# Optimization experiments

Hardware: AMD Instinct MI355X
Metric: run time of the kernel (lower is better)

The kernel has to match this reference:

```python
import jax, jax.numpy as jnp
import numpy as np

N = 500000
E = 500000
F = 128
BN_EPS = 1e-3


def setup_inputs() -> dict:
    key = jax.random.key(0)
    ks = jax.random.split(key, 8)
    return {
        "x": jax.random.normal(ks[0], (N, F), dtype=jnp.float32),
        "pairs_prev": jax.random.randint(ks[1], (E, 2), 0, N, dtype=jnp.int64),
        "pairs_next": jax.random.randint(ks[2], (E, 2), 0, N, dtype=jnp.int64),
        "w_next": jax.random.normal(ks[3], (F, F), dtype=jnp.float32),
        "w_prev": jax.random.normal(ks[4], (F, F), dtype=jnp.float32),
        "b": jnp.zeros((1, F), dtype=jnp.float32),
        "bn_gamma": jnp.ones((F,), dtype=jnp.float32),
        "bn_beta": jnp.zeros((F,), dtype=jnp.float32),
        "gru_kernel": jax.random.normal(ks[5], (F, 3 * F), dtype=jnp.float32) * 0.1,
        "gru_rec_kernel": jax.random.normal(ks[6], (F, 3 * F), dtype=jnp.float32) * 0.1,
        "gru_bias": jax.random.normal(ks[7], (2, 3 * F), dtype=jnp.float32) * 0.1,
    }


def _gru(x, h, kernel, rec_kernel, bias, hidden):
    matrix_x = x @ kernel + bias[0]            # (N, 3H)
    x_z, x_r, x_h = jnp.split(matrix_x, 3, axis=-1)
    matrix_inner = h @ rec_kernel + bias[1]    # (N, 3H)
    rec_z, rec_r, rec_h = jnp.split(matrix_inner, 3, axis=-1)
    z = jax.nn.sigmoid(x_z + rec_z)
    r = jax.nn.sigmoid(x_r + rec_r)
    h_cand = jnp.tanh(x_h + r * rec_h)
    return z * h + (1.0 - z) * h_cand


def reference(x, pairs_prev, pairs_next, w_next, w_prev, b,
              bn_gamma, bn_beta, gru_kernel, gru_rec_kernel, gru_bias):
    num_nodes = x.shape[0]
    # gather source-node features, scatter-add onto target nodes
    prev_sumx = jax.ops.segment_sum(x[pairs_prev[:, 1]], pairs_prev[:, 0],
                                    num_segments=num_nodes)
    next_sumx = jax.ops.segment_sum(x[pairs_next[:, 1]], pairs_next[:, 0],
                                    num_segments=num_nodes)
    aggre = next_sumx @ w_next + prev_sumx @ w_prev + b
    aggre = aggre + x  # multiply=None -> residual skip
    # BatchNorm1d (training mode): batch mean / biased variance over nodes
    a = jax.nn.relu(aggre)
    mean = jnp.mean(a, axis=0)
    var = jnp.mean((a - mean) ** 2, axis=0)
    a = (a - mean) * jax.lax.rsqrt(var + BN_EPS) * bn_gamma + bn_beta
    return _gru(a, x, gru_kernel, gru_rec_kernel, gru_bias, x.shape[1])
```

## Files before the change

kernel.cpp:

```cpp
#include <hip/hip_runtime.h>
#include <hip/hip_bf16.h>

#define N_NODES 500000
#define E_EDGES 500000
#define FDIM 128
#define BN_EPS 1e-3f
#define OFFS 500001
#define GCAP 64

#define WS_BUCKETS 0
#define WS_SCALESHIFT 16384
#define WS_PW 16640
#define WS_PW2 65792
#define WS_XBF 82176

#define SO_CNT 0
#define SO_OFF 1000000
#define SO_PART 2100000
#define SO_CUR 2200000
#define SO_SRC 3200000

typedef __attribute__((ext_vector_type(4))) float v4f;
typedef __attribute__((ext_vector_type(8))) __bf16 v8bf;

__device__ __forceinline__ unsigned f2bf_u(float f) {
  unsigned u = __float_as_uint(f);
  return ((u + 0x7FFF + ((u >> 16) & 1)) >> 16) & 0xFFFF;
}
__device__ __forceinline__ unsigned f2bf2(float a, float b) {
  return f2bf_u(a) | (f2bf_u(b) << 16);
}
__device__ __forceinline__ float bf2f(unsigned short u) {
  return __uint_as_float((unsigned)u << 16);
}
__device__ __forceinline__ float fast_sigmoid(float x) {
  float e = __expf(-x);
  return __builtin_amdgcn_rcpf(1.f + e);
}
__device__ __forceinline__ float fast_tanh(float x) {
  x = fminf(fmaxf(x, -15.f), 15.f);
  float e = __expf(2.f * x);
  return (e - 1.f) * __builtin_amdgcn_rcpf(e + 1.f);
}

__global__ __launch_bounds__(256) void repack_gru(
    const float* __restrict__ gk, const float* __restrict__ rk,
    unsigned short* __restrict__ pw) {
  int idx = blockIdx.x * 256 + threadIdx.x;
  int side = idx / 49152;
  int rem = idx % 49152;
  int gate = rem >> 14;
  int rr = rem & 16383;
  int c = rr >> 7, k = rr & 127;
  const float* src = side ? rk : gk;
  float v = src[k * 384 + gate * 128 + c];
  int w = c >> 5, nb = (c >> 4) & 1, l15 = c & 15;
  int ks = k >> 5, lg = (k >> 3) & 3, j = k & 7;
  int lane = lg * 16 + l15;
  int e = w * 24576 + ks * 6144 + nb * 3072 + gate * 1024 + side * 512 + lane * 8 + j;
  pw[e] = (unsigned short)f2bf_u(v);
}

__global__ __launch_bounds__(256) void repack_w(
    const float* __restrict__ w_next, const float* __restrict__ w_prev,
    unsigned short* __restrict__ pw2) {
  int idx = blockIdx.x * 256 + threadIdx.x;
  int side = idx >> 14;
  int rr = idx & 16383;
  int c = rr >> 7, k = rr & 127;
  const float* src = side ? w_prev : w_next;
  float v = src[k * 128 + c];
  int nh = c >> 6, nb = (c >> 4) & 3, l15 = c & 15;
  int ks = k >> 5, lg = (k >> 3) & 3, j = k & 7;
  int lane = lg * 16 + l15;
  int e = nh * 16384 + ks * 4096 + nb * 1024 + side * 512 + lane * 8 + j;
  pw2[e] = (unsigned short)f2bf_u(v);
}

__global__ __launch_bounds__(256) void xbf_kernel(const float* __restrict__ x,
                                                  unsigned short* __restrict__ xbf) {
  size_t i = ((size_t)blockIdx.x * 256 + threadIdx.x) * 8;
  if (i >= (size_t)N_NODES * FDIM) return;
  float4 a = *(const float4*)(x + i);
  float4 b = *(const float4*)(x + i + 4);
  uint4 o = make_uint4(f2bf2(a.x, a.y), f2bf2(a.z, a.w), f2bf2(b.x, b.y),
                       f2bf2(b.z, b.w));
  *(uint4*)(xbf + i) = o;
}

__global__ __launch_bounds__(256) void hist_kernel(const int* __restrict__ pp,
                                                   const int* __restrict__ pn,
                                                   unsigned* __restrict__ cnt) {
  int i = blockIdx.x * 256 + threadIdx.x;
  if (i >= 2 * E_EDGES) return;
  int side = i >= E_EDGES;
  const int* pair = side ? pn + 2 * (i - E_EDGES) : pp + 2 * i;
  atomicAdd(&cnt[side * N_NODES + pair[0]], 1u);
}

__global__ __launch_bounds__(256) void scan1_kernel(const unsigned* __restrict__ cnt,
                                                    unsigned* __restrict__ off,
                                                    unsigned* __restrict__ part) {
  __shared__ unsigned ls[256];
  int side = blockIdx.y;
  int b = blockIdx.x;
  int td = threadIdx.x;
  int base = b * 1024 + td * 4;
  const unsigned* c = cnt + (size_t)side * N_NODES;
  unsigned v0 = 0, v1 = 0, v2 = 0, v3 = 0;
  if (base + 3 < N_NODES) {
    v0 = c[base]; v1 = c[base + 1]; v2 = c[base + 2]; v3 = c[base + 3];
  } else {
    if (base < N_NODES) v0 = c[base];
    if (base + 1 < N_NODES) v1 = c[base + 1];
    if (base + 2 < N_NODES) v2 = c[base + 2];
  }
  unsigned s = v0 + v1 + v2 + v3;
  ls[td] = s;
  __syncthreads();
  unsigned run = s;
  for (int st = 1; st < 256; st <<= 1) {
    unsigned o = (td >= st) ? ls[td - st] : 0u;
    __syncthreads();
    run += o;
    ls[td] = run;
    __syncthreads();
  }
  unsigned excl = run - s;
  unsigned* oo = off + (size_t)side * OFFS;
  if (base < N_NODES) oo[base] = excl;
  if (base + 1 < N_NODES) oo[base + 1] = excl + v0;
  if (base + 2 < N_NODES) oo[base + 2] = excl + v0 + v1;
  if (base + 3 < N_NODES) oo[base + 3] = excl + v0 + v1 + v2;
  if (td == 255) part[side * 512 + b] = run;
}

__global__ __launch_bounds__(1024) void scan2_kernel(unsigned* __restrict__ part) {
  __shared__ unsigned ls[1024];
  int td = threadIdx.x;
  int b = td & 511;
  unsigned s = part[td];
  ls[td] = s;
  __syncthreads();
  unsigned run = s;
  for (int st = 1; st < 512; st <<= 1) {
    unsigned o = (b >= st) ? ls[td - st] : 0u;
    __syncthreads();
    run += o;
    ls[td] = run;
    __syncthreads();
  }
  part[td] = run - s;
}

__global__ __launch_bounds__(256) void scan3_kernel(unsigned* __restrict__ off,
                                                    const unsigned* __restrict__ part,
                                                    unsigned* __restrict__ cur) {
  int side = blockIdx.y;
  int i = blockIdx.x * 256 + threadIdx.x;
  if (i < N_NODES) {
    unsigned v = off[(size_t)side * OFFS + i] + part[side * 512 + (i >> 10)];
    off[(size_t)side * OFFS + i] = v;
    cur[(size_t)side * N_NODES + i] = v;
  }
  if (i == 0) off[(size_t)side * OFFS + N_NODES] = E_EDGES;
}

__global__ __launch_bounds__(256) void reorder_kernel(const int* __restrict__ pp,
                                                      const int* __restrict__ pn,
                                                      unsigned* __restrict__ cur,
                                                      unsigned* __restrict__ srcbuf) {
  int i = blockIdx.x * 256 + threadIdx.x;
  if (i >= 2 * E_EDGES) return;
  int side = i >= E_EDGES;
  const int* pair = side ? pn + 2 * (i - E_EDGES) : pp + 2 * i;
  unsigned pos = atomicAdd(&cur[(size_t)side * N_NODES + pair[0]], 1u);
  srcbuf[(size_t)side * E_EDGES + pos] = (unsigned)pair[1];
}

__global__ __launch_bounds__(256) void aggre_fused(
    const unsigned short* __restrict__ xbf, const unsigned* __restrict__ off,
    const unsigned* __restrict__ srcbuf, const unsigned short* __restrict__ pw2,
    const float* __restrict__ b, unsigned short* __restrict__ a_out,
    float* __restrict__ buckets) {
  __shared__ unsigned short Ap[32 * 128];
  __shared__ unsigned short An[32 * 128];
  __shared__ unsigned short stage[GCAP][128];
  __shared__ unsigned soff[33];
  __shared__ unsigned ssrc[GCAP];
  __shared__ float rs[2][128];
  __shared__ float rq[2][128];
  int t = threadIdx.x;
  int r0 = blockIdx.x * 32;
  int rr = t >> 3, fc = t & 7;

  for (int side = 0; side < 2; ++side) {
    const unsigned* oo = off + (size_t)side * OFFS + r0;
    if (t < 33) soff[t] = oo[t];
    __syncthreads();
    unsigned e0 = soff[0], e1 = soff[32];
    const unsigned* sl = srcbuf + (size_t)side * E_EDGES;
    float acc[16];
#pragma unroll
    for (int i = 0; i < 16; ++i) acc[i] = 0.f;

    for (unsigned base = e0; base < e1; base += GCAP) {
      unsigned cnt = (e1 - base) < (unsigned)GCAP ? (e1 - base) : (unsigned)GCAP;
      if (t < cnt) ssrc[t] = sl[base + t];
      __syncthreads();
      int g = t >> 5, ld = t & 31;
      for (unsigned j = g; j < cnt; j += 8) {
        size_t s = ssrc[j];
        uint2 v = *(const uint2*)(xbf + s * FDIM + ld * 4);
        *(uint2*)&stage[j][ld * 4] = v;
      }
      __syncthreads();
      unsigned rsb = soff[rr] > base ? soff[rr] : base;
      unsigned reb = soff[rr + 1] < base + cnt ? soff[rr + 1] : base + cnt;
      for (unsigned i = rsb; i < reb; ++i) {
        uint4 u0 = *(const uint4*)&stage[i - base][fc * 16];
        uint4 u1 = *(const uint4*)&stage[i - base][fc * 16 + 8];
        acc[0] += bf2f((unsigned short)(u0.x & 0xffff)); acc[1] += __uint_as_float(u0.x & 0xffff0000u);
        acc[2] += bf2f((unsigned short)(u0.y & 0xffff)); acc[3] += __uint_as_float(u0.y & 0xffff0000u);
        acc[4] += bf2f((unsigned short)(u0.z & 0xffff)); acc[5] += __uint_as_float(u0.z & 0xffff0000u);
        acc[6] += bf2f((unsigned short)(u0.w & 0xffff)); acc[7] += __uint_as_float(u0.w & 0xffff0000u);
        acc[8] += bf2f((unsigned short)(u1.x & 0xffff)); acc[9] += __uint_as_float(u1.x & 0xffff0000u);
        acc[10] += bf2f((unsigned short)(u1.y & 0xffff)); acc[11] += __uint_as_float(u1.y & 0xffff0000u);
        acc[12] += bf2f((unsigned short)(u1.z & 0xffff)); acc[13] += __uint_as_float(u1.z & 0xffff0000u);
        acc[14] += bf2f((unsigned short)(u1.w & 0xffff)); acc[15] += __uint_as_float(u1.w & 0xffff0000u);
      }
      __syncthreads();
    }
    unsigned short* dstl = side ? An : Ap;
    int b0 = (rr * 256 + fc * 32) ^ ((rr & 7) << 4);
    int b1 = (rr * 256 + fc * 32 + 16) ^ ((rr & 7) << 4);
    uint4 o0 = make_uint4(f2bf2(acc[0], acc[1]), f2bf2(acc[2], acc[3]),
                          f2bf2(acc[4], acc[5]), f2bf2(acc[6], acc[7]));
    uint4 o1 = make_uint4(f2bf2(acc[8], acc[9]), f2bf2(acc[10], acc[11]),
                          f2bf2(acc[12], acc[13]), f2bf2(acc[14], acc[15]));
    *(uint4*)((char*)dstl + b0) = o0;
    *(uint4*)((char*)dstl + b1) = o1;
    __syncthreads();
  }

  int w = t >> 6, lane = t & 63;
  int m0 = (w & 1) * 16, nh = w >> 1;
  int l15 = lane & 15, lg = lane >> 4;

  v4f acc[4];
#pragma unroll
  for (int nb = 0; nb < 4; ++nb) acc[nb] = (v4f){0.f, 0.f, 0.f, 0.f};

#pragma unroll
  for (int ks = 0; ks < 4; ++ks) {
    int mm = m0 + l15;
    int byte = (mm * 256 + ks * 64 + lg * 16) ^ ((mm & 7) << 4);
    v8bf ap = __builtin_bit_cast(v8bf, *(const uint4*)((const char*)Ap + byte));
    v8bf an = __builtin_bit_cast(v8bf, *(const uint4*)((const char*)An + byte));
    const unsigned short* wb = pw2 + nh * 16384 + ks * 4096 + lane * 8;
#pragma unroll
    for (int nb = 0; nb < 4; ++nb) {
      v8bf bn_ = __builtin_bit_cast(v8bf, *(const uint4*)(wb + nb * 1024));
      v8bf bp_ = __builtin_bit_cast(v8bf, *(const uint4*)(wb + nb * 1024 + 512));
      acc[nb] = __builtin_amdgcn_mfma_f32_16x16x32_bf16(an, bn_, acc[nb], 0, 0, 0);
      acc[nb] = __builtin_amdgcn_mfma_f32_16x16x32_bf16(ap, bp_, acc[nb], 0, 0, 0);
    }
  }

  float s1[4], s2[4];
#pragma unroll
  for (int nb = 0; nb < 4; ++nb) {
    int c = nh * 64 + nb * 16 + l15;
    float bb = b[c];
    s1[nb] = 0.f;
    s2[nb] = 0.f;
#pragma unroll
    for (int r = 0; r < 4; ++r) {
      int row = r0 + m0 + 4 * lg + r;
      size_t o = (size_t)row * FDIM + c;
      float v = acc[nb][r] + bb + bf2f(xbf[o]);
      v = fmaxf(v, 0.f);
      a_out[o] = (unsigned short)f2bf_u(v);
      s1[nb] += v;
      s2[nb] += v * v;
    }
    s1[nb] += __shfl_xor(s1[nb], 16);
    s1[nb] += __shfl_xor(s1[nb], 32);
    s2[nb] += __shfl_xor(s2[nb], 16);
    s2[nb] += __shfl_xor(s2[nb], 32);
  }
  if (lane < 16) {
#pragma unroll
    for (int nb = 0; nb < 4; ++nb) {
      rs[w & 1][nh * 64 + nb * 16 + lane] = s1[nb];
      rq[w & 1][nh * 64 + nb * 16 + lane] = s2[nb];
    }
  }
  __syncthreads();
  if (t < 128) {
    float s = rs[0][t] + rs[1][t];
    float q = rq[0][t] + rq[1][t];
    float* bkt = buckets + (size_t)(blockIdx.x & 63) * 256;
    atomicAdd(bkt + t, s);
    atomicAdd(bkt + 128 + t, q);
  }
}

__global__ void bn_finalize(const float* __restrict__ buckets,
                            const float* __restrict__ gamma,
                            const float* __restrict__ beta,
                            float* __restrict__ scaleshift) {
  int t = threadIdx.x;
  float s = 0.f, q = 0.f;
  for (int j = 0; j < 64; ++j) {
    s += buckets[j * 256 + t];
    q += buckets[j * 256 + 128 + t];
  }
  float mean = s / (float)N_NODES;
  float var = q / (float)N_NODES - mean * mean;
  var = fmaxf(var, 0.f);
  float sc = gamma[t] * rsqrtf(var + BN_EPS);
  scaleshift[t] = sc;
  scaleshift[128 + t] = beta[t] - mean * sc;
}

__global__ __launch_bounds__(256) void gru_mfma(
    const unsigned short* __restrict__ a_bf, const unsigned short* __restrict__ xbf,
    const unsigned short* __restrict__ pw, const float* __restrict__ gbias,
    const float* __restrict__ scaleshift, float* __restrict__ out) {
  __shared__ unsigned short Aa[32 * 128];
  __shared__ unsigned short Ax[32 * 128];
  int t = threadIdx.x;
  int r0 = blockIdx.x * 32;

#pragma unroll
  for (int i = 0; i < 2; ++i) {
    int q = t + 256 * i;
    int row = q >> 4, kq = q & 15;
    size_t g = (size_t)(r0 + row) * FDIM + kq * 8;
    uint4 av = *(const uint4*)(a_bf + g);
    uint4 xv = *(const uint4*)(xbf + g);
    float4 sc0 = *(const float4*)(scaleshift + kq * 8);
    float4 sc1 = *(const float4*)(scaleshift + kq * 8 + 4);
    float4 sh0 = *(const float4*)(scaleshift + 128 + kq * 8);
    float4 sh1 = *(const float4*)(scaleshift + 128 + kq * 8 + 4);
    float a0 = __uint_as_float(av.x << 16), a1 = __uint_as_float(av.x & 0xffff0000u);
    float a2 = __uint_as_float(av.y << 16), a3 = __uint_as_float(av.y & 0xffff0000u);
    float a4 = __uint_as_float(av.z << 16), a5 = __uint_as_float(av.z & 0xffff0000u);
    float a6 = __uint_as_float(av.w << 16), a7 = __uint_as_float(av.w & 0xffff0000u);
    uint4 na = make_uint4(f2bf2(a0 * sc0.x + sh0.x, a1 * sc0.y + sh0.y),
                          f2bf2(a2 * sc0.z + sh0.z, a3 * sc0.w + sh0.w),
                          f2bf2(a4 * sc1.x + sh1.x, a5 * sc1.y + sh1.y),
                          f2bf2(a6 * sc1.z + sh1.z, a7 * sc1.w + sh1.w));
    int byte = (row * 256 + kq * 16) ^ ((row & 7) << 4);
    *(uint4*)((char*)Aa + byte) = na;
    *(uint4*)((char*)Ax + byte) = xv;
  }
  __syncthreads();

  int w = t >> 6, lane = t & 63;
  int l15 = lane & 15, lg = lane >> 4;

  v4f az[2][2], ar[2][2], ah0[2][2], ah1[2][2];
#pragma unroll
  for (int m = 0; m < 2; ++m)
#pragma unroll
    for (int nb = 0; nb < 2; ++nb) {
      az[m][nb] = (v4f){0.f, 0.f, 0.f, 0.f};
      ar[m][nb] = (v4f){0.f, 0.f, 0.f, 0.f};
      ah0[m][nb] = (v4f){0.f, 0.f, 0.f, 0.f};
      ah1[m][nb] = (v4f){0.f, 0.f, 0.f, 0.f};
    }

#pragma unroll
  for (int ks = 0; ks < 4; ++ks) {
    v8bf aa[2], ax[2];
#pragma unroll
    for (int m = 0; m < 2; ++m) {
      int mm = m * 16 + l15;
      int byte = (mm * 256 + ks * 64 + lg * 16) ^ ((mm & 7) << 4);
      aa[m] = __builtin_bit_cast(v8bf, *(const uint4*)((const char*)Aa + byte));
      ax[m] = __builtin_bit_cast(v8bf, *(const uint4*)((const char*)Ax + byte));
    }
    const unsigned short* wb = pw + w * 24576 + ks * 6144 + lane * 8;
#pragma unroll
    for (int nb = 0; nb < 2; ++nb) {
      const unsigned short* wn = wb + nb * 3072;
      v8bf b0z = __builtin_bit_cast(v8bf, *(const uint4*)(wn));
      v8bf b1z = __builtin_bit_cast(v8bf, *(const uint4*)(wn + 512));
      v8bf b0r = __builtin_bit_cast(v8bf, *(const uint4*)(wn + 1024));
      v8bf b1r = __builtin_bit_cast(v8bf, *(const uint4*)(wn + 1536));
      v8bf b0h = __builtin_bit_cast(v8bf, *(const uint4*)(wn + 2048));
      v8bf b1h = __builtin_bit_cast(v8bf, *(const uint4*)(wn + 2560));
#pragma unroll
      for (int m = 0; m < 2; ++m) {
        az[m][nb] = __builtin_amdgcn_mfma_f32_16x16x32_bf16(aa[m], b0z, az[m][nb], 0, 0, 0);
        az[m][nb] = __builtin_amdgcn_mfma_f32_16x16x32_bf16(ax[m], b1z, az[m][nb], 0, 0, 0);
        ar[m][nb] = __builtin_amdgcn_mfma_f32_16x16x32_bf16(aa[m], b0r, ar[m][nb], 0, 0, 0);
        ar[m][nb] = __builtin_amdgcn_mfma_f32_16x16x32_bf16(ax[m], b1r, ar[m][nb], 0, 0, 0);
        ah0[m][nb] = __builtin_amdgcn_mfma_f32_16x16x32_bf16(aa[m], b0h, ah0[m][nb], 0, 0, 0);
        ah1[m][nb] = __builtin_amdgcn_mfma_f32_16x16x32_bf16(ax[m], b1h, ah1[m][nb], 0, 0, 0);
      }
    }
  }

#pragma unroll
  for (int nb = 0; nb < 2; ++nb) {
    int c = w * 32 + nb * 16 + l15;
    float bz = gbias[c] + gbias[384 + c];
    float br = gbias[128 + c] + gbias[512 + c];
    float bh0 = gbias[256 + c];
    float bh1 = gbias[640 + c];
#pragma unroll
    for (int m = 0; m < 2; ++m) {
#pragma unroll
      for (int r = 0; r < 4; ++r) {
        int rl = m * 16 + 4 * lg + r;
        int row = r0 + rl;
        float z = fast_sigmoid(az[m][nb][r] + bz);
        float rg = fast_sigmoid(ar[m][nb][r] + br);
        float hc = fast_tanh(ah0[m][nb][r] + bh0 + rg * (ah1[m][nb][r] + bh1));
        int hb = (rl * 256 + c * 2) ^ ((rl & 7) << 4);
        float h = bf2f(*(const unsigned short*)((const char*)Ax + hb));
        __builtin_nontemporal_store(z * h + (1.f - z) * hc,
                                    out + (size_t)row * FDIM + c);
      }
    }
  }
}

extern "C" void kernel_launch(void* const* d_in, const int* in_sizes, int n_in,
                              void* d_out, int out_size, void* d_ws, size_t ws_size,
                              hipStream_t stream) {
  const float* x = (const float*)d_in[0];
  const int* pp = (const int*)d_in[1];
  const int* pn = (const int*)d_in[2];
  const float* w_next = (const float*)d_in[3];
  const float* w_prev = (const float*)d_in[4];
  const float* b = (const float*)d_in[5];
  const float* gamma = (const float*)d_in[6];
  const float* beta = (const float*)d_in[7];
  const float* gk = (const float*)d_in[8];
  const float* rk = (const float*)d_in[9];
  const float* gbias = (const float*)d_in[10];
  float* out = (float*)d_out;
  float* ws = (float*)d_ws;

  float* buckets = ws + WS_BUCKETS;
  float* scaleshift = ws + WS_SCALESHIFT;
  unsigned short* pw = (unsigned short*)(ws + WS_PW);
  unsigned short* pw2 = (unsigned short*)(ws + WS_PW2);
  unsigned short* xbf = (unsigned short*)(ws + WS_XBF);
  unsigned short* a_bf = xbf + (size_t)N_NODES * FDIM;

  unsigned* u = (unsigned*)d_out;
  unsigned* cnt = u + SO_CNT;
  unsigned* off = u + SO_OFF;
  unsigned* part = u + SO_PART;
  unsigned* cur = u + SO_CUR;
  unsigned* srcbuf = u + SO_SRC;

  hipMemsetAsync(cnt, 0, 2u * N_NODES * sizeof(unsigned), stream);
  hipMemsetAsync(part, 0, 1024 * sizeof(unsigned), stream);
  hipMemsetAsync(buckets, 0, (16384 + 256) * sizeof(float), stream);

  repack_gru<<<384, 256, 0, stream>>>(gk, rk, pw);
  repack_w<<<128, 256, 0, stream>>>(w_next, w_prev, pw2);
  xbf_kernel<<<31250, 256, 0, stream>>>(x, xbf);

  hist_kernel<<<(2 * E_EDGES + 255) / 256, 256, 0, stream>>>(pp, pn, cnt);
  scan1_kernel<<<dim3(489, 2), 256, 0, stream>>>(cnt, off, part);
  scan2_kernel<<<1, 1024, 0, stream>>>(part);
  scan3_kernel<<<dim3((N_NODES + 255) / 256, 2), 256, 0, stream>>>(off, part, cur);
  reorder_kernel<<<(2 * E_EDGES + 255) / 256, 256, 0, stream>>>(pp, pn, cur, srcbuf);

  aggre_fused<<<N_NODES / 32, 256, 0, stream>>>(xbf, off, srcbuf, pw2, b, a_bf,
                                                buckets);
  bn_finalize<<<1, 128, 0, stream>>>(buckets, gamma, beta, scaleshift);
  gru_mfma<<<N_NODES / 32, 256, 0, stream>>>(a_bf, xbf, pw, gbias, scaleshift, out);
}
```

Measured before the change: 552.1 us.

## Gather neighbor rows directly per thread and fuse histogram into bf16 conversion

The aggregation kernel drops its shared-memory staging of gathered source rows, the chunked index loads and their barriers. Each thread group of 8 now reads the source-row indices for its own node and loads 32-byte slices of each neighbor row straight from global memory into registers. Both sides' offsets are loaded once before the loop, leaving a single barrier ahead of the MFMA stage. The edge histogram is also merged into the x-to-bf16 conversion kernel, saving one launch, at the cost of less coalesced per-row gathers and uneven per-thread work.

```diff
diff --git a/kernel.cpp b/kernel.cpp
--- a/kernel.cpp
+++ b/kernel.cpp
@@ -6,7 +6,6 @@
 #define FDIM 128
 #define BN_EPS 1e-3f
 #define OFFS 500001
-#define GCAP 64
 
 #define WS_BUCKETS 0
 #define WS_SCALESHIFT 16384
@@ -77,25 +76,24 @@
   pw2[e] = (unsigned short)f2bf_u(v);
 }
 
-__global__ __launch_bounds__(256) void xbf_kernel(const float* __restrict__ x,
-                                                  unsigned short* __restrict__ xbf) {
+__global__ __launch_bounds__(256) void xbf_hist_kernel(
+    const float* __restrict__ x, unsigned short* __restrict__ xbf,
+    const int* __restrict__ pp, const int* __restrict__ pn,
+    unsigned* __restrict__ cnt) {
   size_t i = ((size_t)blockIdx.x * 256 + threadIdx.x) * 8;
-  if (i >= (size_t)N_NODES * FDIM) return;
-  float4 a = *(const float4*)(x + i);
-  float4 b = *(const float4*)(x + i + 4);
-  uint4 o = make_uint4(f2bf2(a.x, a.y), f2bf2(a.z, a.w), f2bf2(b.x, b.y),
-                       f2bf2(b.z, b.w));
-  *(uint4*)(xbf + i) = o;
-}
-
-__global__ __launch_bounds__(256) void hist_kernel(const int* __restrict__ pp,
-                                                   const int* __restrict__ pn,
-                                                   unsigned* __restrict__ cnt) {
-  int i = blockIdx.x * 256 + threadIdx.x;
-  if (i >= 2 * E_EDGES) return;
-  int side = i >= E_EDGES;
-  const int* pair = side ? pn + 2 * (i - E_EDGES) : pp + 2 * i;
-  atomicAdd(&cnt[side * N_NODES + pair[0]], 1u);
+  if (i < (size_t)N_NODES * FDIM) {
+    float4 a = *(const float4*)(x + i);
+    float4 b = *(const float4*)(x + i + 4);
+    uint4 o = make_uint4(f2bf2(a.x, a.y), f2bf2(a.z, a.w), f2bf2(b.x, b.y),
+                         f2bf2(b.z, b.w));
+    *(uint4*)(xbf + i) = o;
+  }
+  int e = blockIdx.x * 256 + threadIdx.x;
+  if (e < 2 * E_EDGES) {
+    int side = e >= E_EDGES;
+    const int* pair = side ? pn + 2 * (e - E_EDGES) : pp + 2 * e;
+    atomicAdd(&cnt[side * N_NODES + pair[0]], 1u);
+  }
 }
 
 __global__ __launch_bounds__(256) void scan1_kernel(const unsigned* __restrict__ cnt,
@@ -185,51 +183,38 @@
     float* __restrict__ buckets) {
   __shared__ unsigned short Ap[32 * 128];
   __shared__ unsigned short An[32 * 128];
-  __shared__ unsigned short stage[GCAP][128];
-  __shared__ unsigned soff[33];
-  __shared__ unsigned ssrc[GCAP];
+  __shared__ unsigned soff[2][33];
   __shared__ float rs[2][128];
   __shared__ float rq[2][128];
   int t = threadIdx.x;
   int r0 = blockIdx.x * 32;
   int rr = t >> 3, fc = t & 7;
 
+  if (t < 33) soff[0][t] = off[r0 + t];
+  if (t >= 64 && t < 97) soff[1][t - 64] = off[(size_t)OFFS + r0 + (t - 64)];
+  __syncthreads();
+
+#pragma unroll
   for (int side = 0; side < 2; ++side) {
-    const unsigned* oo = off + (size_t)side * OFFS + r0;
-    if (t < 33) soff[t] = oo[t];
-    __syncthreads();
-    unsigned e0 = soff[0], e1 = soff[32];
+    unsigned s0 = soff[side][rr], s1 = soff[side][rr + 1];
     const unsigned* sl = srcbuf + (size_t)side * E_EDGES;
     float acc[16];
 #pragma unroll
     for (int i = 0; i < 16; ++i) acc[i] = 0.f;
 
-    for (unsigned base = e0; base < e1; base += GCAP) {
-      unsigned cnt = (e1 - base) < (unsigned)GCAP ? (e1 - base) : (unsigned)GCAP;
-      if (t < cnt) ssrc[t] = sl[base + t];
-      __syncthreads();
-      int g = t >> 5, ld = t & 31;
-      for (unsigned j = g; j < cnt; j += 8) {
-        size_t s = ssrc[j];
-        uint2 v = *(const uint2*)(xbf + s * FDIM + ld * 4);
-        *(uint2*)&stage[j][ld * 4] = v;
-      }
-      __syncthreads();
-      unsigned rsb = soff[rr] > base ? soff[rr] : base;
-      unsigned reb = soff[rr + 1] < base + cnt ? soff[rr + 1] : base + cnt;
-      for (unsigned i = rsb; i < reb; ++i) {
-        uint4 u0 = *(const uint4*)&stage[i - base][fc * 16];
-        uint4 u1 = *(const uint4*)&stage[i - base][fc * 16 + 8];
-        acc[0] += bf2f((unsigned short)(u0.x & 0xffff)); acc[1] += __uint_as_float(u0.x & 0xffff0000u);
-        acc[2] += bf2f((unsigned short)(u0.y & 0xffff)); acc[3] += __uint_as_float(u0.y & 0xffff0000u);
-        acc[4] += bf2f((unsigned short)(u0.z & 0xffff)); acc[5] += __uint_as_float(u0.z & 0xffff0000u);
-        acc[6] += bf2f((unsigned short)(u0.w & 0xffff)); acc[7] += __uint_as_float(u0.w & 0xffff0000u);
-        acc[8] += bf2f((unsigned short)(u1.x & 0xffff)); acc[9] += __uint_as_float(u1.x & 0xffff0000u);
-        acc[10] += bf2f((unsigned short)(u1.y & 0xffff)); acc[11] += __uint_as_float(u1.y & 0xffff0000u);
-        acc[12] += bf2f((unsigned short)(u1.z & 0xffff)); acc[13] += __uint_as_float(u1.z & 0xffff0000u);
-        acc[14] += bf2f((unsigned short)(u1.w & 0xffff)); acc[15] += __uint_as_float(u1.w & 0xffff0000u);
-      }
-      __syncthreads();
+    for (unsigned i = s0; i < s1; ++i) {
+      size_t s = sl[i];
+      const unsigned short* p = xbf + s * FDIM + fc * 16;
+      uint4 u0 = *(const uint4*)p;
+      uint4 u1 = *(const uint4*)(p + 8);
+      acc[0] += bf2f((unsigned short)(u0.x & 0xffff)); acc[1] += __uint_as_float(u0.x & 0xffff0000u);
+      acc[2] += bf2f((unsigned short)(u0.y & 0xffff)); acc[3] += __uint_as_float(u0.y & 0xffff0000u);
+      acc[4] += bf2f((unsigned short)(u0.z & 0xffff)); acc[5] += __uint_as_float(u0.z & 0xffff0000u);
+      acc[6] += bf2f((unsigned short)(u0.w & 0xffff)); acc[7] += __uint_as_float(u0.w & 0xffff0000u);
+      acc[8] += bf2f((unsigned short)(u1.x & 0xffff)); acc[9] += __uint_as_float(u1.x & 0xffff0000u);
+      acc[10] += bf2f((unsigned short)(u1.y & 0xffff)); acc[11] += __uint_as_float(u1.y & 0xffff0000u);
+      acc[12] += bf2f((unsigned short)(u1.z & 0xffff)); acc[13] += __uint_as_float(u1.z & 0xffff0000u);
+      acc[14] += bf2f((unsigned short)(u1.w & 0xffff)); acc[15] += __uint_as_float(u1.w & 0xffff0000u);
     }
     unsigned short* dstl = side ? An : Ap;
     int b0 = (rr * 256 + fc * 32) ^ ((rr & 7) << 4);
@@ -240,8 +225,8 @@
                           f2bf2(acc[12], acc[13]), f2bf2(acc[14], acc[15]));
     *(uint4*)((char*)dstl + b0) = o0;
     *(uint4*)((char*)dstl + b1) = o1;
-    __syncthreads();
-  }
+  }
+  __syncthreads();
 
   int w = t >> 6, lane = t & 63;
   int m0 = (w & 1) * 16, nh = w >> 1;
@@ -466,9 +451,8 @@
 
   repack_gru<<<384, 256, 0, stream>>>(gk, rk, pw);
   repack_w<<<128, 256, 0, stream>>>(w_next, w_prev, pw2);
-  xbf_kernel<<<31250, 256, 0, stream>>>(x, xbf);
-
-  hist_kernel<<<(2 * E_EDGES + 255) / 256, 256, 0, stream>>>(pp, pn, cnt);
+  xbf_hist_kernel<<<31250, 256, 0, stream>>>(x, xbf, pp, pn, cnt);
+
   scan1_kernel<<<dim3(489, 2), 256, 0, stream>>>(cnt, off, part);
   scan2_kernel<<<1, 1024, 0, stream>>>(part);
   scan3_kernel<<<dim3((N_NODES + 255) / 256, 2), 256, 0, stream>>>(off, part, cur);
```

Measured after the change: 509.1 us. 1.08x faster.
